# Performance work log

Hardware: AMD Instinct MI355X
Metric: run time of the kernel (lower is better)

The kernel has to match this reference:

```python
import jax, jax.numpy as jnp
import numpy as np

B, N, E, C = 8, 4096, 1024, 512


def setup_inputs() -> dict:
    key = jax.random.key(0)
    k1, k2, k3, k4 = jax.random.split(key, 4)
    node_feats = jax.random.normal(k1, (B, N, C), dtype=jnp.float32)
    hyper_feats = jax.random.normal(k2, (B, E, C), dtype=jnp.float32)
    # torch nn.Linear params: weight [out, in], bias [out]
    Wq = jax.random.normal(k3, (C, C), dtype=jnp.float32) * (1.0 / np.sqrt(C))
    bq = jnp.zeros((C,), dtype=jnp.float32)
    Wkv = jax.random.normal(k4, (2 * C, C), dtype=jnp.float32) * (1.0 / np.sqrt(C))
    bkv = jnp.zeros((2 * C,), dtype=jnp.float32)
    return {"node_feats": node_feats, "hyper_feats": hyper_feats,
            "Wq": Wq, "bq": bq, "Wkv": Wkv, "bkv": bkv}


def reference(node_feats, hyper_feats, Wq, bq, Wkv, bkv):
    C_ = node_feats.shape[-1]
    scale = C_ ** -0.5
    Q = node_feats @ Wq.T + bq                      # [B,N,C]
    KV = hyper_feats @ Wkv.T + bkv                  # [B,E,2C]
    K, V = KV[..., :C_], KV[..., C_:]               # [B,E,C] each
    attn = jnp.einsum('bnc,bec->bne', Q, K) * scale  # [B,N,E]
    attn = jax.nn.softmax(attn, axis=-1)
    return jnp.einsum('bne,bec->bnc', attn, V)       # [B,N,C]
```

## Files before the change

kernel.cpp:

```cpp
#include <hip/hip_runtime.h>
#include <cstdint>
#include <cstddef>

typedef _Float16 h16;
typedef _Float16 h16x4 __attribute__((ext_vector_type(4)));
typedef _Float16 h16x8 __attribute__((ext_vector_type(8)));
typedef float fx4 __attribute__((ext_vector_type(4)));

static constexpr int B_ = 8, N_ = 4096, E_ = 1024, C_ = 512;
static constexpr float SCALE = 0.044194173824159216f;

__device__ __forceinline__ void glds16(const h16* g, h16* l) {
  __builtin_amdgcn_global_load_lds(
      (const __attribute__((address_space(1))) unsigned int*)g,
      (__attribute__((address_space(3))) unsigned int*)l, 16, 0, 0);
}

__global__ __launch_bounds__(256) void cvt_kernel(const float* __restrict__ src,
                                                  h16* __restrict__ dst, int n8) {
  int i = blockIdx.x * 256 + threadIdx.x;
  if (i >= n8) return;
  const float4* s4 = (const float4*)src;
  float4 a = s4[2 * i], b = s4[2 * i + 1];
  h16x8 o;
  o[0] = (h16)a.x; o[1] = (h16)a.y; o[2] = (h16)a.z; o[3] = (h16)a.w;
  o[4] = (h16)b.x; o[5] = (h16)b.y; o[6] = (h16)b.z; o[7] = (h16)b.w;
  *(h16x8*)(dst + (size_t)i * 8) = o;
}

template <int MODE>
__global__ __launch_bounds__(512) void gemm256(
    const h16* __restrict__ A, const h16* __restrict__ Bm,
    const float* __restrict__ bias,
    h16* __restrict__ outH, h16* __restrict__ outK, h16* __restrict__ outVt,
    float* __restrict__ outF, float* __restrict__ rowsum,
    int Ncols, int K) {
  extern __shared__ h16 lds[];
  const int tid = threadIdx.x;
  const int wave = tid >> 6, lane = tid & 63;
  const int wm = wave >> 2, wn = wave & 3;
  const int lr = lane & 15, kq = lane >> 4;
  const int mBase = blockIdx.x * 256, nBase = blockIdx.y * 256;
  const int z = blockIdx.z;
  if (MODE == 2) { A += (size_t)z * N_ * C_; Bm += (size_t)z * E_ * C_;
                   outH += (size_t)z * N_ * E_; rowsum += (size_t)z * N_; }
  if (MODE == 3) { A += (size_t)z * N_ * E_; Bm += (size_t)z * C_ * E_;
                   outF += (size_t)z * N_ * C_; rowsum += (size_t)z * N_; }

  fx4 acc[8][4];
#pragma unroll
  for (int i = 0; i < 8; ++i)
#pragma unroll
    for (int j = 0; j < 4; ++j) acc[i][j] = (fx4){0.f, 0.f, 0.f, 0.f};

  float bv[4] = {0.f, 0.f, 0.f, 0.f};
  if constexpr (MODE <= 1) {
#pragma unroll
    for (int ni = 0; ni < 4; ++ni) bv[ni] = bias[nBase + wn * 64 + ni * 16 + lr];
  }

  int aoff[8], boff[4];
#pragma unroll
  for (int f = 0; f < 8; ++f) {
    int row = wm * 128 + f * 16 + lr;
    int r2 = row >> 1;
    int s8 = (((row & 1) << 2) | kq) ^ (r2 & 7);
    aoff[f] = r2 * 64 + s8 * 8;
  }
#pragma unroll
  for (int n = 0; n < 4; ++n) {
    int row = wn * 64 + n * 16 + lr;
    int r2 = row >> 1;
    int s8 = (((row & 1) << 2) | kq) ^ (r2 & 7);
    boff[n] = 8192 + r2 * 64 + s8 * 8;
  }

  size_t aSrc[2], bSrc[2];
#pragma unroll
  for (int i = 0; i < 2; ++i) {
    int r2 = i * 64 + (tid >> 3);
    int so8 = (tid & 7) ^ (r2 & 7);
    int grow = 2 * r2 + (so8 >> 2);
    int gcol = (so8 & 3) * 8;
    aSrc[i] = (size_t)(mBase + grow) * K + gcol;
    bSrc[i] = (size_t)(nBase + grow) * K + gcol;
  }
  const int KH = K >> 5, SU = KH * 2;

  auto stage = [&](int s) {
    int kh2 = s >> 1;
    h16* lb = lds + (kh2 & 3) * 16384 + (s & 1) * 8192 + wave * 512;
    int kc = kh2 * 32;
    if ((s & 1) == 0) {
      glds16(A + aSrc[0] + kc, lb);
      glds16(A + aSrc[1] + kc, lb + 4096);
    } else {
      glds16(Bm + bSrc[0] + kc, lb);
      glds16(Bm + bSrc[1] + kc, lb + 4096);
    }
  };

#pragma unroll
  for (int s = 0; s < 5; ++s) stage(s);
  asm volatile("s_waitcnt vmcnt(6)" ::: "memory");
  __builtin_amdgcn_s_barrier();

  int s_next = 5;
  for (int kh = 0; kh < KH; ++kh) {
    const int sb = (kh & 3) * 16384;
    h16x8 af[4], bf[4];
#pragma unroll
    for (int i = 0; i < 4; ++i) af[i] = *(const h16x8*)&lds[sb + aoff[i]];
#pragma unroll
    for (int i = 0; i < 4; ++i) bf[i] = *(const h16x8*)&lds[sb + boff[i]];
    if (s_next < SU) stage(s_next);
    ++s_next;
    __builtin_amdgcn_s_barrier();
    asm volatile("s_waitcnt lgkmcnt(0)" ::: "memory");
    __builtin_amdgcn_sched_barrier(0);
    __builtin_amdgcn_s_setprio(1);
#pragma unroll
    for (int mi = 0; mi < 4; ++mi)
#pragma unroll
      for (int ni = 0; ni < 4; ++ni)
        acc[mi][ni] = __builtin_amdgcn_mfma_f32_16x16x32_f16(af[mi], bf[ni],
                                                             acc[mi][ni], 0, 0, 0);
    __builtin_amdgcn_s_setprio(0);
    __builtin_amdgcn_s_barrier();
#pragma unroll
    for (int i = 0; i < 4; ++i) af[i] = *(const h16x8*)&lds[sb + aoff[4 + i]];
    if (s_next < SU) stage(s_next);
    ++s_next;
    asm volatile("s_waitcnt vmcnt(6)" ::: "memory");
    __builtin_amdgcn_s_barrier();
    asm volatile("s_waitcnt lgkmcnt(0)" ::: "memory");
    __builtin_amdgcn_sched_barrier(0);
    __builtin_amdgcn_s_setprio(1);
#pragma unroll
    for (int mi = 0; mi < 4; ++mi)
#pragma unroll
      for (int ni = 0; ni < 4; ++ni)
        acc[4 + mi][ni] = __builtin_amdgcn_mfma_f32_16x16x32_f16(af[mi], bf[ni],
                                                                 acc[4 + mi][ni], 0, 0, 0);
    __builtin_amdgcn_s_setprio(0);
    __builtin_amdgcn_s_barrier();
  }

  const int rbase = kq * 4;
  if (MODE == 2) {
#pragma unroll
    for (int mi = 0; mi < 8; ++mi) {
#pragma unroll
      for (int r = 0; r < 4; ++r) {
        int row = mBase + wm * 128 + mi * 16 + rbase + r;
        float rs = 0.f;
#pragma unroll
        for (int ni = 0; ni < 4; ++ni) {
          int col = nBase + wn * 64 + ni * 16 + lr;
          float e = __expf(acc[mi][ni][r] * SCALE);
          rs += e;
          outH[(size_t)row * Ncols + col] = (h16)e;
        }
        rs += __shfl_xor(rs, 1); rs += __shfl_xor(rs, 2);
        rs += __shfl_xor(rs, 4); rs += __shfl_xor(rs, 8);
        if (lr == 0) atomicAdd(&rowsum[row], rs);
      }
    }
  } else if (MODE == 3) {
#pragma unroll
    for (int mi = 0; mi < 8; ++mi) {
#pragma unroll
      for (int r = 0; r < 4; ++r) {
        int row = mBase + wm * 128 + mi * 16 + rbase + r;
        float inv = 1.0f / rowsum[row];
#pragma unroll
        for (int ni = 0; ni < 4; ++ni) {
          int col = nBase + wn * 64 + ni * 16 + lr;
          outF[(size_t)row * Ncols + col] = acc[mi][ni][r] * inv;
        }
      }
    }
  } else {
#pragma unroll
    for (int mi = 0; mi < 8; ++mi) {
      int row0 = mBase + wm * 128 + mi * 16 + rbase;
#pragma unroll
      for (int ni = 0; ni < 4; ++ni) {
        int col = nBase + wn * 64 + ni * 16 + lr;
        if (MODE == 1 && col >= C_) {
          h16x4 pk;
#pragma unroll
          for (int r = 0; r < 4; ++r) pk[r] = (h16)(acc[mi][ni][r] + bv[ni]);
          int zb = row0 >> 10, e = row0 & 1023;
          *(h16x4*)&outVt[((size_t)zb * C_ + (col - C_)) * E_ + e] = pk;
        } else {
#pragma unroll
          for (int r = 0; r < 4; ++r) {
            float v = acc[mi][ni][r] + bv[ni];
            if (MODE == 0) outH[(size_t)(row0 + r) * Ncols + col] = (h16)v;
            else           outK[(size_t)(row0 + r) * C_ + col] = (h16)v;
          }
        }
      }
    }
  }
}

extern "C" void kernel_launch(void* const* d_in, const int* in_sizes, int n_in,
                              void* d_out, int out_size, void* d_ws, size_t ws_size,
                              hipStream_t stream) {
  const float* node  = (const float*)d_in[0];
  const float* hyper = (const float*)d_in[1];
  const float* Wq    = (const float*)d_in[2];
  const float* bq    = (const float*)d_in[3];
  const float* Wkv   = (const float*)d_in[4];
  const float* bkv   = (const float*)d_in[5];
  float* out = (float*)d_out;
  char* ws = (char*)d_ws;

  h16* S_h     = (h16*)(ws + 0);
  h16* node_h  = (h16*)(ws + 0);
  h16* hyper_h = (h16*)(ws + 33554432);
  h16* Q_h     = (h16*)(ws + 67108864);
  h16* K_h     = (h16*)(ws + 100663296);
  h16* Vt_h    = (h16*)(ws + 109051904);
  h16* Wq_h    = (h16*)(ws + 117440512);
  h16* Wkv_h   = (h16*)(ws + 117964800);
  float* rowsum = (float*)(ws + 119013376);
  if (ws_size < 119144448u) return;

  static int attr_done = 0;
  if (!attr_done) {
    hipFuncSetAttribute(reinterpret_cast<const void*>(&gemm256<0>),
                        hipFuncAttributeMaxDynamicSharedMemorySize, 131072);
    hipFuncSetAttribute(reinterpret_cast<const void*>(&gemm256<1>),
                        hipFuncAttributeMaxDynamicSharedMemorySize, 131072);
    hipFuncSetAttribute(reinterpret_cast<const void*>(&gemm256<2>),
                        hipFuncAttributeMaxDynamicSharedMemorySize, 131072);
    hipFuncSetAttribute(reinterpret_cast<const void*>(&gemm256<3>),
                        hipFuncAttributeMaxDynamicSharedMemorySize, 131072);
    attr_done = 1;
  }

  cvt_kernel<<<dim3(C_ * C_ / 8 / 256), 256, 0, stream>>>(Wq, Wq_h, C_ * C_ / 8);
  cvt_kernel<<<dim3(2 * C_ * C_ / 8 / 256), 256, 0, stream>>>(Wkv, Wkv_h, 2 * C_ * C_ / 8);
  cvt_kernel<<<dim3(B_ * N_ * C_ / 8 / 256), 256, 0, stream>>>(node, node_h, B_ * N_ * C_ / 8);
  cvt_kernel<<<dim3(B_ * E_ * C_ / 8 / 256), 256, 0, stream>>>(hyper, hyper_h, B_ * E_ * C_ / 8);
  hipMemsetAsync(rowsum, 0, (size_t)B_ * N_ * sizeof(float), stream);

  gemm256<0><<<dim3(B_ * N_ / 256, C_ / 256), 512, 131072, stream>>>(
      node_h, Wq_h, bq, Q_h, nullptr, nullptr, nullptr, nullptr, C_, C_);
  gemm256<1><<<dim3(B_ * E_ / 256, 2 * C_ / 256), 512, 131072, stream>>>(
      hyper_h, Wkv_h, bkv, nullptr, K_h, Vt_h, nullptr, nullptr, 2 * C_, C_);
  gemm256<2><<<dim3(N_ / 256, E_ / 256, B_), 512, 131072, stream>>>(
      Q_h, K_h, nullptr, S_h, nullptr, nullptr, nullptr, rowsum, E_, C_);
  gemm256<3><<<dim3(N_ / 256, C_ / 256, B_), 512, 131072, stream>>>(
      S_h, Vt_h, nullptr, nullptr, nullptr, nullptr, out, rowsum, C_, E_);
}
```

Measured before the change: 289.9 us.

## Shrink GEMM tile to 128x256 with 3-stage LDS ring and higher occupancy

```diff
diff --git a/kernel.cpp b/kernel.cpp
--- a/kernel.cpp
+++ b/kernel.cpp
@@ -29,7 +29,7 @@
 }
 
 template <int MODE>
-__global__ __launch_bounds__(512) void gemm256(
+__global__ __launch_bounds__(512, 4) void gemm128(
     const h16* __restrict__ A, const h16* __restrict__ Bm,
     const float* __restrict__ bias,
     h16* __restrict__ outH, h16* __restrict__ outK, h16* __restrict__ outVt,
@@ -40,29 +40,23 @@
   const int wave = tid >> 6, lane = tid & 63;
   const int wm = wave >> 2, wn = wave & 3;
   const int lr = lane & 15, kq = lane >> 4;
-  const int mBase = blockIdx.x * 256, nBase = blockIdx.y * 256;
+  const int mBase = blockIdx.x * 128, nBase = blockIdx.y * 256;
   const int z = blockIdx.z;
   if (MODE == 2) { A += (size_t)z * N_ * C_; Bm += (size_t)z * E_ * C_;
                    outH += (size_t)z * N_ * E_; rowsum += (size_t)z * N_; }
   if (MODE == 3) { A += (size_t)z * N_ * E_; Bm += (size_t)z * C_ * E_;
                    outF += (size_t)z * N_ * C_; rowsum += (size_t)z * N_; }
 
-  fx4 acc[8][4];
-#pragma unroll
-  for (int i = 0; i < 8; ++i)
+  fx4 acc[4][4];
+#pragma unroll
+  for (int i = 0; i < 4; ++i)
 #pragma unroll
     for (int j = 0; j < 4; ++j) acc[i][j] = (fx4){0.f, 0.f, 0.f, 0.f};
 
-  float bv[4] = {0.f, 0.f, 0.f, 0.f};
-  if constexpr (MODE <= 1) {
-#pragma unroll
-    for (int ni = 0; ni < 4; ++ni) bv[ni] = bias[nBase + wn * 64 + ni * 16 + lr];
-  }
-
-  int aoff[8], boff[4];
-#pragma unroll
-  for (int f = 0; f < 8; ++f) {
-    int row = wm * 128 + f * 16 + lr;
+  int aoff[4], boff[4];
+#pragma unroll
+  for (int f = 0; f < 4; ++f) {
+    int row = wm * 64 + f * 16 + lr;
     int r2 = row >> 1;
     int s8 = (((row & 1) << 2) | kq) ^ (r2 & 7);
     aoff[f] = r2 * 64 + s8 * 8;
@@ -72,49 +66,50 @@
     int row = wn * 64 + n * 16 + lr;
     int r2 = row >> 1;
     int s8 = (((row & 1) << 2) | kq) ^ (r2 & 7);
-    boff[n] = 8192 + r2 * 64 + s8 * 8;
-  }
-
-  size_t aSrc[2], bSrc[2];
+    boff[n] = 4096 + r2 * 64 + s8 * 8;
+  }
+
+  unsigned aS, bS[2];
+  {
+    int r2 = tid >> 3;
+    int so8 = (tid & 7) ^ (r2 & 7);
+    aS = (unsigned)((mBase + 2 * r2 + (so8 >> 2)) * K + (so8 & 3) * 8);
+  }
 #pragma unroll
   for (int i = 0; i < 2; ++i) {
     int r2 = i * 64 + (tid >> 3);
     int so8 = (tid & 7) ^ (r2 & 7);
-    int grow = 2 * r2 + (so8 >> 2);
-    int gcol = (so8 & 3) * 8;
-    aSrc[i] = (size_t)(mBase + grow) * K + gcol;
-    bSrc[i] = (size_t)(nBase + grow) * K + gcol;
-  }
-  const int KH = K >> 5, SU = KH * 2;
-
-  auto stage = [&](int s) {
-    int kh2 = s >> 1;
-    h16* lb = lds + (kh2 & 3) * 16384 + (s & 1) * 8192 + wave * 512;
-    int kc = kh2 * 32;
-    if ((s & 1) == 0) {
-      glds16(A + aSrc[0] + kc, lb);
-      glds16(A + aSrc[1] + kc, lb + 4096);
+    bS[i] = (unsigned)((nBase + 2 * r2 + (so8 >> 2)) * K + (so8 & 3) * 8);
+  }
+  const int KH = K >> 5;
+
+  auto stage = [&](int kh, int si) {
+    h16* slot = lds + si * 12288;
+    int kc = kh * 32;
+    glds16(A + aS + kc, slot + wave * 512);
+    glds16(Bm + bS[0] + kc, slot + 4096 + wave * 512);
+    glds16(Bm + bS[1] + kc, slot + 8192 + wave * 512);
+  };
+
+  stage(0, 0);
+  stage(1, 1);
+  asm volatile("s_waitcnt vmcnt(3)" ::: "memory");
+  __builtin_amdgcn_s_barrier();
+
+  int siR = 0, siS = 2;
+  for (int kh = 0; kh < KH; ++kh) {
+    const int sb = siR * 12288;
+    h16x8 af[4], bf[4];
+#pragma unroll
+    for (int i = 0; i < 4; ++i) af[i] = *(const h16x8*)&lds[sb + aoff[i]];
+#pragma unroll
+    for (int i = 0; i < 4; ++i) bf[i] = *(const h16x8*)&lds[sb + boff[i]];
+    if (kh + 2 < KH) stage(kh + 2, siS);
+    if (kh < KH - 2) {
+      asm volatile("s_waitcnt vmcnt(3)" ::: "memory");
     } else {
-      glds16(Bm + bSrc[0] + kc, lb);
-      glds16(Bm + bSrc[1] + kc, lb + 4096);
-    }
-  };
-
-#pragma unroll
-  for (int s = 0; s < 5; ++s) stage(s);
-  asm volatile("s_waitcnt vmcnt(6)" ::: "memory");
-  __builtin_amdgcn_s_barrier();
-
-  int s_next = 5;
-  for (int kh = 0; kh < KH; ++kh) {
-    const int sb = (kh & 3) * 16384;
-    h16x8 af[4], bf[4];
-#pragma unroll
-    for (int i = 0; i < 4; ++i) af[i] = *(const h16x8*)&lds[sb + aoff[i]];
-#pragma unroll
-    for (int i = 0; i < 4; ++i) bf[i] = *(const h16x8*)&lds[sb + boff[i]];
-    if (s_next < SU) stage(s_next);
-    ++s_next;
+      asm volatile("s_waitcnt vmcnt(0)" ::: "memory");
+    }
     __builtin_amdgcn_s_barrier();
     asm volatile("s_waitcnt lgkmcnt(0)" ::: "memory");
     __builtin_amdgcn_sched_barrier(0);
@@ -127,32 +122,17 @@
                                                              acc[mi][ni], 0, 0, 0);
     __builtin_amdgcn_s_setprio(0);
     __builtin_amdgcn_s_barrier();
-#pragma unroll
-    for (int i = 0; i < 4; ++i) af[i] = *(const h16x8*)&lds[sb + aoff[4 + i]];
-    if (s_next < SU) stage(s_next);
-    ++s_next;
-    asm volatile("s_waitcnt vmcnt(6)" ::: "memory");
-    __builtin_amdgcn_s_barrier();
-    asm volatile("s_waitcnt lgkmcnt(0)" ::: "memory");
-    __builtin_amdgcn_sched_barrier(0);
-    __builtin_amdgcn_s_setprio(1);
-#pragma unroll
-    for (int mi = 0; mi < 4; ++mi)
-#pragma unroll
-      for (int ni = 0; ni < 4; ++ni)
-        acc[4 + mi][ni] = __builtin_amdgcn_mfma_f32_16x16x32_f16(af[mi], bf[ni],
-                                                                 acc[4 + mi][ni], 0, 0, 0);
-    __builtin_amdgcn_s_setprio(0);
-    __builtin_amdgcn_s_barrier();
+    siR = (siR == 2) ? 0 : siR + 1;
+    siS = (siS == 2) ? 0 : siS + 1;
   }
 
   const int rbase = kq * 4;
   if (MODE == 2) {
 #pragma unroll
-    for (int mi = 0; mi < 8; ++mi) {
+    for (int mi = 0; mi < 4; ++mi) {
 #pragma unroll
       for (int r = 0; r < 4; ++r) {
-        int row = mBase + wm * 128 + mi * 16 + rbase + r;
+        int row = mBase + wm * 64 + mi * 16 + rbase + r;
         float rs = 0.f;
 #pragma unroll
         for (int ni = 0; ni < 4; ++ni) {
@@ -168,10 +148,10 @@
     }
   } else if (MODE == 3) {
 #pragma unroll
-    for (int mi = 0; mi < 8; ++mi) {
+    for (int mi = 0; mi < 4; ++mi) {
 #pragma unroll
       for (int r = 0; r < 4; ++r) {
-        int row = mBase + wm * 128 + mi * 16 + rbase + r;
+        int row = mBase + wm * 64 + mi * 16 + rbase + r;
         float inv = 1.0f / rowsum[row];
 #pragma unroll
         for (int ni = 0; ni < 4; ++ni) {
@@ -181,9 +161,12 @@
       }
     }
   } else {
-#pragma unroll
-    for (int mi = 0; mi < 8; ++mi) {
-      int row0 = mBase + wm * 128 + mi * 16 + rbase;
+    float bv[4];
+#pragma unroll
+    for (int ni = 0; ni < 4; ++ni) bv[ni] = bias[nBase + wn * 64 + ni * 16 + lr];
+#pragma unroll
+    for (int mi = 0; mi < 4; ++mi) {
+      int row0 = mBase + wm * 64 + mi * 16 + rbase;
 #pragma unroll
       for (int ni = 0; ni < 4; ++ni) {
         int col = nBase + wn * 64 + ni * 16 + lr;
@@ -231,14 +214,14 @@
 
   static int attr_done = 0;
   if (!attr_done) {
-    hipFuncSetAttribute(reinterpret_cast<const void*>(&gemm256<0>),
-                        hipFuncAttributeMaxDynamicSharedMemorySize, 131072);
-    hipFuncSetAttribute(reinterpret_cast<const void*>(&gemm256<1>),
-                        hipFuncAttributeMaxDynamicSharedMemorySize, 131072);
-    hipFuncSetAttribute(reinterpret_cast<const void*>(&gemm256<2>),
-                        hipFuncAttributeMaxDynamicSharedMemorySize, 131072);
-    hipFuncSetAttribute(reinterpret_cast<const void*>(&gemm256<3>),
-                        hipFuncAttributeMaxDynamicSharedMemorySize, 131072);
+    hipFuncSetAttribute(reinterpret_cast<const void*>(&gemm128<0>),
+                        hipFuncAttributeMaxDynamicSharedMemorySize, 73728);
+    hipFuncSetAttribute(reinterpret_cast<const void*>(&gemm128<1>),
+                        hipFuncAttributeMaxDynamicSharedMemorySize, 73728);
+    hipFuncSetAttribute(reinterpret_cast<const void*>(&gemm128<2>),
+                        hipFuncAttributeMaxDynamicSharedMemorySize, 73728);
+    hipFuncSetAttribute(reinterpret_cast<const void*>(&gemm128<3>),
+                        hipFuncAttributeMaxDynamicSharedMemorySize, 73728);
     attr_done = 1;
   }
 
@@ -248,12 +231,12 @@
   cvt_kernel<<<dim3(B_ * E_ * C_ / 8 / 256), 256, 0, stream>>>(hyper, hyper_h, B_ * E_ * C_ / 8);
   hipMemsetAsync(rowsum, 0, (size_t)B_ * N_ * sizeof(float), stream);
 
-  gemm256<0><<<dim3(B_ * N_ / 256, C_ / 256), 512, 131072, stream>>>(
+  gemm128<0><<<dim3(B_ * N_ / 128, C_ / 256), 512, 73728, stream>>>(
       node_h, Wq_h, bq, Q_h, nullptr, nullptr, nullptr, nullptr, C_, C_);
-  gemm256<1><<<dim3(B_ * E_ / 256, 2 * C_ / 256), 512, 131072, stream>>>(
+  gemm128<1><<<dim3(B_ * E_ / 128, 2 * C_ / 256), 512, 73728, stream>>>(
       hyper_h, Wkv_h, bkv, nullptr, K_h, Vt_h, nullptr, nullptr, 2 * C_, C_);
-  gemm256<2><<<dim3(N_ / 256, E_ / 256, B_), 512, 131072, stream>>>(
+  gemm128<2><<<dim3(N_ / 128, E_ / 256, B_), 512, 73728, stream>>>(
       Q_h, K_h, nullptr, S_h, nullptr, nullptr, nullptr, rowsum, E_, C_);
-  gemm256<3><<<dim3(N_ / 256, C_ / 256, B_), 512, 131072, stream>>>(
+  gemm128<3><<<dim3(N_ / 128, C_ / 256, B_), 512, 73728, stream>>>(
       S_h, Vt_h, nullptr, nullptr, nullptr, nullptr, out, rowsum, C_, E_);
 }
```

Measured after the change: 272.2 us. 6.1% less time.

## Deepen GEMM prefetch pipeline, swizzle block order, use 32-bit offsets

Applied to the files above, without the earlier changes.

```diff
diff --git a/kernel.cpp b/kernel.cpp
--- a/kernel.cpp
+++ b/kernel.cpp
@@ -36,12 +36,19 @@
     float* __restrict__ outF, float* __restrict__ rowsum,
     int Ncols, int K) {
   extern __shared__ h16 lds[];
+  const int gx = gridDim.x, gy = gridDim.y;
+  int id = blockIdx.x + gx * (blockIdx.y + gy * blockIdx.z);
+  int cpx = (gx * gy * (int)gridDim.z) >> 3;
+  int swz = (id & 7) * cpx + (id >> 3);
+  int bx = swz % gx, t_ = swz / gx;
+  int by = t_ % gy, bz = t_ / gy;
+
   const int tid = threadIdx.x;
   const int wave = tid >> 6, lane = tid & 63;
   const int wm = wave >> 2, wn = wave & 3;
   const int lr = lane & 15, kq = lane >> 4;
-  const int mBase = blockIdx.x * 256, nBase = blockIdx.y * 256;
-  const int z = blockIdx.z;
+  const int mBase = bx * 256, nBase = by * 256;
+  const int z = bz;
   if (MODE == 2) { A += (size_t)z * N_ * C_; Bm += (size_t)z * E_ * C_;
                    outH += (size_t)z * N_ * E_; rowsum += (size_t)z * N_; }
   if (MODE == 3) { A += (size_t)z * N_ * E_; Bm += (size_t)z * C_ * E_;
@@ -52,12 +59,6 @@
   for (int i = 0; i < 8; ++i)
 #pragma unroll
     for (int j = 0; j < 4; ++j) acc[i][j] = (fx4){0.f, 0.f, 0.f, 0.f};
-
-  float bv[4] = {0.f, 0.f, 0.f, 0.f};
-  if constexpr (MODE <= 1) {
-#pragma unroll
-    for (int ni = 0; ni < 4; ++ni) bv[ni] = bias[nBase + wn * 64 + ni * 16 + lr];
-  }
 
   int aoff[8], boff[4];
 #pragma unroll
@@ -75,37 +76,37 @@
     boff[n] = 8192 + r2 * 64 + s8 * 8;
   }
 
-  size_t aSrc[2], bSrc[2];
+  unsigned aSrc[2], bSrc[2];
 #pragma unroll
   for (int i = 0; i < 2; ++i) {
     int r2 = i * 64 + (tid >> 3);
     int so8 = (tid & 7) ^ (r2 & 7);
     int grow = 2 * r2 + (so8 >> 2);
     int gcol = (so8 & 3) * 8;
-    aSrc[i] = (size_t)(mBase + grow) * K + gcol;
-    bSrc[i] = (size_t)(nBase + grow) * K + gcol;
-  }
-  const int KH = K >> 5, SU = KH * 2;
-
-  auto stage = [&](int s) {
-    int kh2 = s >> 1;
-    h16* lb = lds + (kh2 & 3) * 16384 + (s & 1) * 8192 + wave * 512;
-    int kc = kh2 * 32;
-    if ((s & 1) == 0) {
-      glds16(A + aSrc[0] + kc, lb);
-      glds16(A + aSrc[1] + kc, lb + 4096);
-    } else {
-      glds16(Bm + bSrc[0] + kc, lb);
-      glds16(Bm + bSrc[1] + kc, lb + 4096);
-    }
+    aSrc[i] = (unsigned)((mBase + grow) * K + gcol);
+    bSrc[i] = (unsigned)((nBase + grow) * K + gcol);
+  }
+  const int KH = K >> 5;
+
+  auto stageA = [&](int kh) {
+    h16* lb = lds + (kh & 3) * 16384 + wave * 512;
+    int kc = kh * 32;
+    glds16(A + aSrc[0] + kc, lb);
+    glds16(A + aSrc[1] + kc, lb + 4096);
   };
-
-#pragma unroll
-  for (int s = 0; s < 5; ++s) stage(s);
-  asm volatile("s_waitcnt vmcnt(6)" ::: "memory");
+  auto stageB = [&](int kh) {
+    h16* lb = lds + (kh & 3) * 16384 + 8192 + wave * 512;
+    int kc = kh * 32;
+    glds16(Bm + bSrc[0] + kc, lb);
+    glds16(Bm + bSrc[1] + kc, lb + 4096);
+  };
+
+  stageA(0); stageB(0);
+  stageA(1); stageB(1);
+  stageA(2); stageB(2);
+  asm volatile("s_waitcnt vmcnt(8)" ::: "memory");
   __builtin_amdgcn_s_barrier();
 
-  int s_next = 5;
   for (int kh = 0; kh < KH; ++kh) {
     const int sb = (kh & 3) * 16384;
     h16x8 af[4], bf[4];
@@ -113,8 +114,7 @@
     for (int i = 0; i < 4; ++i) af[i] = *(const h16x8*)&lds[sb + aoff[i]];
 #pragma unroll
     for (int i = 0; i < 4; ++i) bf[i] = *(const h16x8*)&lds[sb + boff[i]];
-    if (s_next < SU) stage(s_next);
-    ++s_next;
+    if (kh + 3 < KH) stageA(kh + 3);
     __builtin_amdgcn_s_barrier();
     asm volatile("s_waitcnt lgkmcnt(0)" ::: "memory");
     __builtin_amdgcn_sched_barrier(0);
@@ -129,9 +129,10 @@
     __builtin_amdgcn_s_barrier();
 #pragma unroll
     for (int i = 0; i < 4; ++i) af[i] = *(const h16x8*)&lds[sb + aoff[4 + i]];
-    if (s_next < SU) stage(s_next);
-    ++s_next;
-    asm volatile("s_waitcnt vmcnt(6)" ::: "memory");
+    if (kh + 3 < KH) stageB(kh + 3);
+    if (kh < KH - 3)       { asm volatile("s_waitcnt vmcnt(8)" ::: "memory"); }
+    else if (kh == KH - 3) { asm volatile("s_waitcnt vmcnt(4)" ::: "memory"); }
+    else                   { asm volatile("s_waitcnt vmcnt(0)" ::: "memory"); }
     __builtin_amdgcn_s_barrier();
     asm volatile("s_waitcnt lgkmcnt(0)" ::: "memory");
     __builtin_amdgcn_sched_barrier(0);
@@ -181,6 +182,9 @@
       }
     }
   } else {
+    float bv[4];
+#pragma unroll
+    for (int ni = 0; ni < 4; ++ni) bv[ni] = bias[nBase + wn * 64 + ni * 16 + lr];
 #pragma unroll
     for (int mi = 0; mi < 8; ++mi) {
       int row0 = mBase + wm * 128 + mi * 16 + rbase;
```

New measurement: 288.5 us. Within noise of the previous version (-0.5%).
